# Optimization experiments

Measured on AMD Instinct MI355X. Metric: run time of the kernel, lower is better.

Reference implementation:

```python
import jax, jax.numpy as jnp
import numpy as np

B, L, D = 8, 1024, 512
H, Qd = 8, 64  # heads, per-head dim (q == v == 64)


def setup_inputs() -> dict:
    key = jax.random.key(0)
    ks = jax.random.split(key, 12)
    s = 0.02
    return {
        "x": jax.random.normal(ks[0], (B, L, D), dtype=jnp.float32),
        # Conv1d(D, D, kernel_size=1) == pointwise linear over channels
        "Wc": jax.random.normal(ks[1], (D, D), dtype=jnp.float32) * s,
        "bc": jax.random.normal(ks[2], (D,), dtype=jnp.float32) * s,
        "Wq": jax.random.normal(ks[3], (H * Qd, D), dtype=jnp.float32) * s,
        "bq": jax.random.normal(ks[4], (H * Qd,), dtype=jnp.float32) * s,
        "Wk": jax.random.normal(ks[5], (H * Qd, D), dtype=jnp.float32) * s,
        "bk": jax.random.normal(ks[6], (H * Qd,), dtype=jnp.float32) * s,
        "Wv": jax.random.normal(ks[7], (H * Qd, D), dtype=jnp.float32) * s,
        "bv": jax.random.normal(ks[8], (H * Qd,), dtype=jnp.float32) * s,
        "Wo": jax.random.normal(ks[9], (D, H * Qd), dtype=jnp.float32) * s,
        "bo": jax.random.normal(ks[10], (D,), dtype=jnp.float32) * s,
    }


def reference(x, Wc, bc, Wq, bq, Wk, bk, Wv, bv, Wo, bo):
    b, l, d = x.shape
    # kernel-size-1 Conv1d over channel dim == per-position linear
    x_r = jnp.einsum('bld,od->blo', x, Wc) + bc  # [B, L, D], Lr == L
    Q = (x @ Wq.T + bq).reshape(b, l, H, Qd).transpose(0, 2, 1, 3)    # bhld
    K = (x_r @ Wk.T + bk).reshape(b, l, H, Qd).transpose(0, 2, 1, 3)  # bhjd
    V = (x_r @ Wv.T + bv).reshape(b, l, H, Qd).transpose(0, 2, 1, 3)  # bhjd
    scores = jax.nn.softmax(
        jnp.einsum('bhld,bhjd->bhlj', Q, K) / np.sqrt(Qd).astype(np.float32),
        axis=-1)  # [B, H, L, L] — returned explicitly, must be materialized
    atten = jnp.einsum('bhlj,bhjd->bhld', scores, V)
    # NB: original flattens as (d, h), not the usual (h, d)
    merged = atten.transpose(0, 2, 3, 1).reshape(b, l, H * Qd)
    out = merged @ Wo.T + bo  # [B, L, D]
    return (out, scores)
```

## Files before the change

### kernel.cpp

```cpp
#include <hip/hip_runtime.h>
#include <stdint.h>

#define DEV __device__ __forceinline__

typedef __attribute__((ext_vector_type(8))) short short8;
typedef __attribute__((ext_vector_type(4))) float floatx4;

DEV ushort f2bf(float f) {
  union { float f; uint32_t u; } v; v.f = f;
  uint32_t u = v.u;
  return (ushort)((u + 0x7fffu + ((u >> 16) & 1u)) >> 16);
}

DEV float bf2f(ushort u) {
  union { uint32_t u; float f; } v; v.u = ((uint32_t)u) << 16;
  return v.f;
}

DEV floatx4 zero4() { floatx4 v; v[0] = 0.f; v[1] = 0.f; v[2] = 0.f; v[3] = 0.f; return v; }

__global__ __launch_bounds__(256) void cast_all(
    const float* __restrict__ x,
    const float* __restrict__ Wc, const float* __restrict__ Wq,
    const float* __restrict__ Wk, const float* __restrict__ Wv,
    const float* __restrict__ Wo,
    ushort* __restrict__ xb,
    ushort* __restrict__ Wcb, ushort* __restrict__ Wqb,
    ushort* __restrict__ Wkb, ushort* __restrict__ Wvb,
    ushort* __restrict__ Wob)
{
  const int y = blockIdx.y;
  const int i4 = blockIdx.x * 256 + threadIdx.x;
  if (y == 0) {
    if (i4 >= 1048576) return;
    float4 v = ((const float4*)x)[i4];
    ushort4 o;
    o.x = f2bf(v.x); o.y = f2bf(v.y); o.z = f2bf(v.z); o.w = f2bf(v.w);
    *(ushort4*)&xb[i4 * 4] = o;
  } else if (y <= 4) {
    if (i4 >= 65536) return;
    const float* s = (y == 1) ? Wc : (y == 2) ? Wq : (y == 3) ? Wk : Wv;
    ushort* d = (y == 1) ? Wcb : (y == 2) ? Wqb : (y == 3) ? Wkb : Wvb;
    float4 v = ((const float4*)s)[i4];
    ushort4 o;
    o.x = f2bf(v.x); o.y = f2bf(v.y); o.z = f2bf(v.z); o.w = f2bf(v.w);
    *(ushort4*)&d[i4 * 4] = o;
  } else {
    if (i4 >= 65536) return;
    int base = i4 * 4;
    #pragma unroll
    for (int k = 0; k < 4; k++) {
      int e = base + k;
      int o = e >> 9;
      int hd = e & 511;
      int h = hd >> 6, qd = hd & 63;
      Wob[e] = f2bf(Wo[o * 512 + qd * 8 + h]);
    }
  }
}

template <typename OutT>
__global__ __launch_bounds__(256) void gemm_bias(
    const ushort* __restrict__ A, int lda,
    const ushort* __restrict__ W,
    const float* __restrict__ bias0, const float* __restrict__ bias1,
    OutT* __restrict__ C, int ldc)
{
  __shared__ ushort As[64 * 40];
  __shared__ ushort Bs[64 * 40];

  const int t = threadIdx.x;
  const int lane = t & 63, w = t >> 6;
  const int ln = lane & 15, q = lane >> 4;
  const int row0 = blockIdx.y * 64, col0 = blockIdx.x * 64;
  const int wm = w >> 1, wn = w & 1;

  floatx4 acc[2][2];
  #pragma unroll
  for (int i = 0; i < 2; i++)
    #pragma unroll
    for (int j = 0; j < 2; j++) acc[i][j] = zero4();

  const int sr = t >> 2, ss = t & 3;
  for (int k0 = 0; k0 < 512; k0 += 32) {
    *(short8*)&As[sr * 40 + ss * 8] =
        *(const short8*)&A[(size_t)(row0 + sr) * lda + k0 + ss * 8];
    *(short8*)&Bs[sr * 40 + ss * 8] =
        *(const short8*)&W[(size_t)(col0 + sr) * 512 + k0 + ss * 8];
    __syncthreads();
    short8 af[2], bf[2];
    #pragma unroll
    for (int mi = 0; mi < 2; mi++)
      af[mi] = *(const short8*)&As[(wm * 32 + mi * 16 + ln) * 40 + q * 8];
    #pragma unroll
    for (int ni = 0; ni < 2; ni++)
      bf[ni] = *(const short8*)&Bs[(wn * 32 + ni * 16 + ln) * 40 + q * 8];
    #pragma unroll
    for (int mi = 0; mi < 2; mi++)
      #pragma unroll
      for (int ni = 0; ni < 2; ni++)
        acc[mi][ni] = __builtin_amdgcn_mfma_f32_16x16x32_bf16(
            af[mi], bf[ni], acc[mi][ni], 0, 0, 0);
    __syncthreads();
  }

  #pragma unroll
  for (int mi = 0; mi < 2; mi++)
    #pragma unroll
    for (int ni = 0; ni < 2; ni++) {
      int gcol = col0 + wn * 32 + ni * 16 + ln;
      float bv = (gcol < 512) ? bias0[gcol] : bias1[gcol - 512];
      #pragma unroll
      for (int r = 0; r < 4; r++) {
        int grow = row0 + wm * 32 + mi * 16 + q * 4 + r;
        float val = acc[mi][ni][r] + bv;
        if constexpr (sizeof(OutT) == 2) {
          C[(size_t)grow * ldc + gcol] = (OutT)f2bf(val);
        } else {
          C[(size_t)grow * ldc + gcol] = (OutT)val;
        }
      }
    }
}

__global__ __launch_bounds__(256) void vtrans(
    const ushort* __restrict__ KV, ushort* __restrict__ Vt)
{
  __shared__ ushort Ts[64 * 72];
  const int t = threadIdx.x;
  const int lt = blockIdx.x, pair = blockIdx.y;
  const int b = pair >> 3, h = pair & 7;
  #pragma unroll
  for (int i = 0; i < 2; i++) {
    int e = t + i * 256;
    int r = e >> 3, s = e & 7;
    *(short8*)&Ts[r * 72 + s * 8] =
        *(const short8*)&KV[((size_t)b * 1024 + lt * 64 + r) * 1024 + 512 + h * 64 + s * 8];
  }
  __syncthreads();
  #pragma unroll
  for (int i = 0; i < 2; i++) {
    int e = t + i * 256;
    int d = e >> 3, s = e & 7;
    short8 o;
    #pragma unroll
    for (int k = 0; k < 8; k++) o[k] = (short)Ts[(s * 8 + k) * 72 + d];
    *(short8*)&Vt[((size_t)pair * 64 + d) * 1024 + lt * 64 + s * 8] = o;
  }
}

__global__ __launch_bounds__(512) void attn(
    const ushort* __restrict__ XQ,
    const ushort* __restrict__ KV,
    const ushort* __restrict__ Vt,
    float* __restrict__ scores,
    ushort* __restrict__ Ab)
{
  __shared__ ushort Stage[128 * 72];
  __shared__ ushort Ps[32 * 136];
  __shared__ float sm[128];
  __shared__ float sl[128];

  const int t = threadIdx.x;
  const int lane = t & 63, w = t >> 6;
  const int ln = lane & 15, q = lane >> 4;
  const int wr = w >> 2, wc = w & 3;
  const int rt = blockIdx.x, pair = blockIdx.y;
  const int b = pair >> 3, h = pair & 7;
  const int l0 = rt * 32;
  const size_t bRow = (size_t)b * 1024;

  const ushort* qrow = &XQ[(bRow + l0 + wr * 16 + ln) * 1024 + 512 + h * 64];
  short8 a0 = *(const short8*)&qrow[q * 8];
  short8 a1 = *(const short8*)&qrow[32 + q * 8];

  floatx4 S[16];
  #pragma unroll
  for (int i = 0; i < 16; i++) S[i] = zero4();

  for (int ch = 0; ch < 8; ch++) {
    #pragma unroll
    for (int i = 0; i < 2; i++) {
      int e = t + i * 512;
      int r = e >> 3, s = e & 7;
      *(short8*)&Stage[r * 72 + s * 8] =
          *(const short8*)&KV[(bRow + ch * 128 + r) * 1024 + h * 64 + s * 8];
    }
    __syncthreads();
    #pragma unroll
    for (int sub = 0; sub < 2; sub++) {
      int jr = (wc + sub * 4) * 16;
      short8 b0 = *(const short8*)&Stage[(jr + ln) * 72 + q * 8];
      short8 b1 = *(const short8*)&Stage[(jr + ln) * 72 + 32 + q * 8];
      int ct = ch * 2 + sub;
      S[ct] = __builtin_amdgcn_mfma_f32_16x16x32_bf16(a0, b0, S[ct], 0, 0, 0);
      S[ct] = __builtin_amdgcn_mfma_f32_16x16x32_bf16(a1, b1, S[ct], 0, 0, 0);
    }
    __syncthreads();
  }

  float mr[4];
  #pragma unroll
  for (int r = 0; r < 4; r++) {
    float m = -3.4e38f;
    #pragma unroll
    for (int ct = 0; ct < 16; ct++) m = fmaxf(m, S[ct][r]);
    #pragma unroll
    for (int off = 1; off < 16; off <<= 1) m = fmaxf(m, __shfl_xor(m, off));
    mr[r] = m;
  }
  if (ln == 0) {
    #pragma unroll
    for (int r = 0; r < 4; r++) sm[wr * 64 + wc * 16 + q * 4 + r] = mr[r];
  }
  __syncthreads();
  float mfull[4], lsum[4];
  #pragma unroll
  for (int r = 0; r < 4; r++) {
    int base = wr * 64 + q * 4 + r;
    mfull[r] = fmaxf(fmaxf(sm[base], sm[base + 16]),
                     fmaxf(sm[base + 32], sm[base + 48]));
    lsum[r] = 0.0f;
  }
  #pragma unroll
  for (int ct = 0; ct < 16; ct++)
    #pragma unroll
    for (int r = 0; r < 4; r++) {
      float e = __expf((S[ct][r] - mfull[r]) * 0.125f);
      S[ct][r] = e;
      lsum[r] += e;
    }
  #pragma unroll
  for (int r = 0; r < 4; r++) {
    #pragma unroll
    for (int off = 1; off < 16; off <<= 1) lsum[r] += __shfl_xor(lsum[r], off);
  }
  if (ln == 0) {
    #pragma unroll
    for (int r = 0; r < 4; r++) sl[wr * 64 + wc * 16 + q * 4 + r] = lsum[r];
  }
  __syncthreads();
  float rl[4];
  #pragma unroll
  for (int r = 0; r < 4; r++) {
    int base = wr * 64 + q * 4 + r;
    rl[r] = 1.0f / (sl[base] + sl[base + 16] + sl[base + 32] + sl[base + 48]);
  }

  floatx4 O = zero4();
  const int srow = t >> 4;
  const int scb = (t & 15) * 8;
  for (int ch = 0; ch < 8; ch++) {
    #pragma unroll
    for (int i = 0; i < 2; i++) {
      int e = t + i * 512;
      int r = e >> 4, s = e & 15;
      *(short8*)&Stage[r * 136 + s * 8] =
          *(const short8*)&Vt[((size_t)pair * 64 + r) * 1024 + ch * 128 + s * 8];
    }
    #pragma unroll
    for (int sub = 0; sub < 2; sub++) {
      int ct = ch * 2 + sub;
      int c0 = (wc + sub * 4) * 16;
      #pragma unroll
      for (int r = 0; r < 4; r++)
        Ps[(wr * 16 + q * 4 + r) * 136 + c0 + ln] = f2bf(S[ct][r] * rl[r]);
    }
    __syncthreads();
    {
      short8 pv = *(const short8*)&Ps[srow * 136 + scb];
      size_t so = ((size_t)pair * 1024 + l0 + srow) * 1024 + ch * 128 + scb;
      float4 f0, f1;
      f0.x = bf2f((ushort)pv[0]); f0.y = bf2f((ushort)pv[1]);
      f0.z = bf2f((ushort)pv[2]); f0.w = bf2f((ushort)pv[3]);
      f1.x = bf2f((ushort)pv[4]); f1.y = bf2f((ushort)pv[5]);
      f1.z = bf2f((ushort)pv[6]); f1.w = bf2f((ushort)pv[7]);
      *(float4*)&scores[so] = f0;
      *(float4*)&scores[so + 4] = f1;
    }
    #pragma unroll
    for (int kc = 0; kc < 4; kc++) {
      short8 af = *(const short8*)&Ps[(wr * 16 + ln) * 136 + kc * 32 + q * 8];
      short8 bf = *(const short8*)&Stage[(wc * 16 + ln) * 136 + kc * 32 + q * 8];
      O = __builtin_amdgcn_mfma_f32_16x16x32_bf16(af, bf, O, 0, 0, 0);
    }
    __syncthreads();
  }

  #pragma unroll
  for (int r = 0; r < 4; r++) {
    Ab[(bRow + l0 + wr * 16 + q * 4 + r) * 512 + h * 64 + wc * 16 + ln] = f2bf(O[r]);
  }
}

extern "C" void kernel_launch(void* const* d_in, const int* in_sizes, int n_in,
                              void* d_out, int out_size, void* d_ws, size_t ws_size,
                              hipStream_t stream)
{
  const float* x  = (const float*)d_in[0];
  const float* Wc = (const float*)d_in[1];
  const float* bc = (const float*)d_in[2];
  const float* Wq = (const float*)d_in[3];
  const float* bq = (const float*)d_in[4];
  const float* Wk = (const float*)d_in[5];
  const float* bk = (const float*)d_in[6];
  const float* Wv = (const float*)d_in[7];
  const float* bv = (const float*)d_in[8];
  const float* Wo = (const float*)d_in[9];
  const float* bo = (const float*)d_in[10];

  float* out = (float*)d_out;
  float* scores = out + (size_t)8 * 1024 * 512;

  char* ws = (char*)d_ws;
  const size_t MB = (size_t)1 << 20;
  ushort* xb  = (ushort*)(ws + 0);
  ushort* Ab  = xb;
  ushort* XQ  = (ushort*)(ws + 8 * MB);
  ushort* KV  = (ushort*)(ws + 24 * MB);
  ushort* Vt  = (ushort*)(ws + 40 * MB);
  ushort* W1  = (ushort*)(ws + 48 * MB);
  ushort* W2  = (ushort*)(ws + 49 * MB);
  ushort* Wob = (ushort*)(ws + 50 * MB);

  cast_all<<<dim3(4096, 6), 256, 0, stream>>>(
      x, Wc, Wq, Wk, Wv, Wo,
      xb, W1, W1 + 262144, W2, W2 + 262144, Wob);

  gemm_bias<ushort><<<dim3(16, 128), 256, 0, stream>>>(
      xb, 512, W1, bc, bq, XQ, 1024);
  gemm_bias<ushort><<<dim3(16, 128), 256, 0, stream>>>(
      XQ, 1024, W2, bk, bv, KV, 1024);

  vtrans<<<dim3(16, 64), 256, 0, stream>>>(KV, Vt);

  attn<<<dim3(32, 64), 512, 0, stream>>>(XQ, KV, Vt, scores, Ab);

  gemm_bias<float><<<dim3(8, 128), 256, 0, stream>>>(
      Ab, 512, Wob, bo, bo, out, 512);
}
```

Before: 429.6 us.

## Retile GEMMs to 128x128 with swizzled LDS and restructure attention to direct-load K/V

The GEMM kernel moves to 128x128 tiles with a 64-wide K step and XOR-swizzled shared memory, giving more reuse per load and fewer bank conflicts. The attention kernel drops LDS staging for K and V and reads them straight from global memory into MFMA operands. It writes fp32 scores directly with nontemporal stores, before bf16 rounding, and keeps the full probability row block in a swizzled 64KB LDS buffer. Grid order is swapped so blocks sharing a head run together, and the cast kernel uses a flat grid with no idle blocks. The larger LDS footprint in attention lowers occupancy, and uncoalesced direct K/V loads may cost bandwidth.

```diff
diff --git a/kernel.cpp b/kernel.cpp
--- a/kernel.cpp
+++ b/kernel.cpp
@@ -10,11 +10,6 @@
   union { float f; uint32_t u; } v; v.f = f;
   uint32_t u = v.u;
   return (ushort)((u + 0x7fffu + ((u >> 16) & 1u)) >> 16);
-}
-
-DEV float bf2f(ushort u) {
-  union { uint32_t u; float f; } v; v.u = ((uint32_t)u) << 16;
-  return v.f;
 }
 
 DEV floatx4 zero4() { floatx4 v; v[0] = 0.f; v[1] = 0.f; v[2] = 0.f; v[3] = 0.f; return v; }
@@ -29,16 +24,20 @@
     ushort* __restrict__ Wkb, ushort* __restrict__ Wvb,
     ushort* __restrict__ Wob)
 {
-  const int y = blockIdx.y;
-  const int i4 = blockIdx.x * 256 + threadIdx.x;
+  const int bx = blockIdx.x;
+  int y, i4;
+  if (bx < 4096) { y = 0; i4 = bx * 256 + threadIdx.x; }
+  else {
+    int e = bx - 4096;
+    y = 1 + (e >> 8);
+    i4 = (e & 255) * 256 + threadIdx.x;
+  }
   if (y == 0) {
-    if (i4 >= 1048576) return;
     float4 v = ((const float4*)x)[i4];
     ushort4 o;
     o.x = f2bf(v.x); o.y = f2bf(v.y); o.z = f2bf(v.z); o.w = f2bf(v.w);
     *(ushort4*)&xb[i4 * 4] = o;
   } else if (y <= 4) {
-    if (i4 >= 65536) return;
     const float* s = (y == 1) ? Wc : (y == 2) ? Wq : (y == 3) ? Wk : Wv;
     ushort* d = (y == 1) ? Wcb : (y == 2) ? Wqb : (y == 3) ? Wkb : Wvb;
     float4 v = ((const float4*)s)[i4];
@@ -46,7 +45,6 @@
     o.x = f2bf(v.x); o.y = f2bf(v.y); o.z = f2bf(v.z); o.w = f2bf(v.w);
     *(ushort4*)&d[i4 * 4] = o;
   } else {
-    if (i4 >= 65536) return;
     int base = i4 * 4;
     #pragma unroll
     for (int k = 0; k < 4; k++) {
@@ -66,53 +64,67 @@
     const float* __restrict__ bias0, const float* __restrict__ bias1,
     OutT* __restrict__ C, int ldc)
 {
-  __shared__ ushort As[64 * 40];
-  __shared__ ushort Bs[64 * 40];
+  __shared__ __align__(16) ushort As[128 * 64];
+  __shared__ __align__(16) ushort Bs[128 * 64];
 
   const int t = threadIdx.x;
-  const int lane = t & 63, w = t >> 6;
+  const int lane = t & 63;
   const int ln = lane & 15, q = lane >> 4;
-  const int row0 = blockIdx.y * 64, col0 = blockIdx.x * 64;
+  const int w = t >> 6;
   const int wm = w >> 1, wn = w & 1;
-
-  floatx4 acc[2][2];
-  #pragma unroll
-  for (int i = 0; i < 2; i++)
-    #pragma unroll
-    for (int j = 0; j < 2; j++) acc[i][j] = zero4();
-
-  const int sr = t >> 2, ss = t & 3;
-  for (int k0 = 0; k0 < 512; k0 += 32) {
-    *(short8*)&As[sr * 40 + ss * 8] =
-        *(const short8*)&A[(size_t)(row0 + sr) * lda + k0 + ss * 8];
-    *(short8*)&Bs[sr * 40 + ss * 8] =
-        *(const short8*)&W[(size_t)(col0 + sr) * 512 + k0 + ss * 8];
+  const int row0 = blockIdx.x * 128, col0 = blockIdx.y * 128;
+
+  floatx4 acc[4][4];
+  #pragma unroll
+  for (int i = 0; i < 4; i++)
+    #pragma unroll
+    for (int j = 0; j < 4; j++) acc[i][j] = zero4();
+
+  const char* asb = (const char*)As;
+  const char* bsb = (const char*)Bs;
+
+  for (int k0 = 0; k0 < 512; k0 += 64) {
+    #pragma unroll
+    for (int i = 0; i < 4; i++) {
+      int L = i * 256 + t;
+      int r = L >> 3, s = L & 7;
+      int sg = s ^ (r & 7);
+      *(short8*)&As[L * 8] = *(const short8*)&A[(size_t)(row0 + r) * lda + k0 + sg * 8];
+      *(short8*)&Bs[L * 8] = *(const short8*)&W[(size_t)(col0 + r) * 512 + k0 + sg * 8];
+    }
     __syncthreads();
-    short8 af[2], bf[2];
-    #pragma unroll
-    for (int mi = 0; mi < 2; mi++)
-      af[mi] = *(const short8*)&As[(wm * 32 + mi * 16 + ln) * 40 + q * 8];
-    #pragma unroll
-    for (int ni = 0; ni < 2; ni++)
-      bf[ni] = *(const short8*)&Bs[(wn * 32 + ni * 16 + ln) * 40 + q * 8];
-    #pragma unroll
-    for (int mi = 0; mi < 2; mi++)
+    #pragma unroll
+    for (int kk = 0; kk < 2; kk++) {
+      short8 af[4], bf[4];
       #pragma unroll
-      for (int ni = 0; ni < 2; ni++)
-        acc[mi][ni] = __builtin_amdgcn_mfma_f32_16x16x32_bf16(
-            af[mi], bf[ni], acc[mi][ni], 0, 0, 0);
+      for (int mi = 0; mi < 4; mi++) {
+        int row = wm * 64 + mi * 16 + ln;
+        af[mi] = *(const short8*)(asb + ((row * 128 + kk * 64 + q * 16) ^ ((row & 7) << 4)));
+      }
+      #pragma unroll
+      for (int ni = 0; ni < 4; ni++) {
+        int row = wn * 64 + ni * 16 + ln;
+        bf[ni] = *(const short8*)(bsb + ((row * 128 + kk * 64 + q * 16) ^ ((row & 7) << 4)));
+      }
+      #pragma unroll
+      for (int mi = 0; mi < 4; mi++)
+        #pragma unroll
+        for (int ni = 0; ni < 4; ni++)
+          acc[mi][ni] = __builtin_amdgcn_mfma_f32_16x16x32_bf16(
+              af[mi], bf[ni], acc[mi][ni], 0, 0, 0);
+    }
     __syncthreads();
   }
 
   #pragma unroll
-  for (int mi = 0; mi < 2; mi++)
-    #pragma unroll
-    for (int ni = 0; ni < 2; ni++) {
-      int gcol = col0 + wn * 32 + ni * 16 + ln;
+  for (int mi = 0; mi < 4; mi++)
+    #pragma unroll
+    for (int ni = 0; ni < 4; ni++) {
+      int gcol = col0 + wn * 64 + ni * 16 + ln;
       float bv = (gcol < 512) ? bias0[gcol] : bias1[gcol - 512];
       #pragma unroll
       for (int r = 0; r < 4; r++) {
-        int grow = row0 + wm * 32 + mi * 16 + q * 4 + r;
+        int grow = row0 + wm * 64 + mi * 16 + q * 4 + r;
         float val = acc[mi][ni][r] + bv;
         if constexpr (sizeof(OutT) == 2) {
           C[(size_t)grow * ldc + gcol] = (OutT)f2bf(val);
@@ -126,7 +138,7 @@
 __global__ __launch_bounds__(256) void vtrans(
     const ushort* __restrict__ KV, ushort* __restrict__ Vt)
 {
-  __shared__ ushort Ts[64 * 72];
+  __shared__ __align__(16) ushort Ts[64 * 72];
   const int t = threadIdx.x;
   const int lt = blockIdx.x, pair = blockIdx.y;
   const int b = pair >> 3, h = pair & 7;
@@ -156,8 +168,7 @@
     float* __restrict__ scores,
     ushort* __restrict__ Ab)
 {
-  __shared__ ushort Stage[128 * 72];
-  __shared__ ushort Ps[32 * 136];
+  __shared__ __align__(16) ushort Ps[32 * 1024];
   __shared__ float sm[128];
   __shared__ float sl[128];
 
@@ -165,7 +176,7 @@
   const int lane = t & 63, w = t >> 6;
   const int ln = lane & 15, q = lane >> 4;
   const int wr = w >> 2, wc = w & 3;
-  const int rt = blockIdx.x, pair = blockIdx.y;
+  const int pair = blockIdx.x, rt = blockIdx.y;
   const int b = pair >> 3, h = pair & 7;
   const int l0 = rt * 32;
   const size_t bRow = (size_t)b * 1024;
@@ -178,25 +189,14 @@
   #pragma unroll
   for (int i = 0; i < 16; i++) S[i] = zero4();
 
-  for (int ch = 0; ch < 8; ch++) {
-    #pragma unroll
-    for (int i = 0; i < 2; i++) {
-      int e = t + i * 512;
-      int r = e >> 3, s = e & 7;
-      *(short8*)&Stage[r * 72 + s * 8] =
-          *(const short8*)&KV[(bRow + ch * 128 + r) * 1024 + h * 64 + s * 8];
-    }
-    __syncthreads();
-    #pragma unroll
-    for (int sub = 0; sub < 2; sub++) {
-      int jr = (wc + sub * 4) * 16;
-      short8 b0 = *(const short8*)&Stage[(jr + ln) * 72 + q * 8];
-      short8 b1 = *(const short8*)&Stage[(jr + ln) * 72 + 32 + q * 8];
-      int ct = ch * 2 + sub;
-      S[ct] = __builtin_amdgcn_mfma_f32_16x16x32_bf16(a0, b0, S[ct], 0, 0, 0);
-      S[ct] = __builtin_amdgcn_mfma_f32_16x16x32_bf16(a1, b1, S[ct], 0, 0, 0);
-    }
-    __syncthreads();
+  const ushort* krow = &KV[(bRow + wc * 16 + ln) * 1024 + h * 64];
+  #pragma unroll
+  for (int ct = 0; ct < 16; ct++) {
+    const ushort* kp = krow + (size_t)ct * 64 * 1024;
+    short8 b0 = *(const short8*)&kp[q * 8];
+    short8 b1 = *(const short8*)&kp[32 + q * 8];
+    S[ct] = __builtin_amdgcn_mfma_f32_16x16x32_bf16(a0, b0, S[ct], 0, 0, 0);
+    S[ct] = __builtin_amdgcn_mfma_f32_16x16x32_bf16(a1, b1, S[ct], 0, 0, 0);
   }
 
   float mr[4];
@@ -247,49 +247,41 @@
     rl[r] = 1.0f / (sl[base] + sl[base + 16] + sl[base + 32] + sl[base + 48]);
   }
 
-  floatx4 O = zero4();
-  const int srow = t >> 4;
-  const int scb = (t & 15) * 8;
-  for (int ch = 0; ch < 8; ch++) {
-    #pragma unroll
-    for (int i = 0; i < 2; i++) {
-      int e = t + i * 512;
-      int r = e >> 4, s = e & 15;
-      *(short8*)&Stage[r * 136 + s * 8] =
-          *(const short8*)&Vt[((size_t)pair * 64 + r) * 1024 + ch * 128 + s * 8];
-    }
-    #pragma unroll
-    for (int sub = 0; sub < 2; sub++) {
-      int ct = ch * 2 + sub;
-      int c0 = (wc + sub * 4) * 16;
-      #pragma unroll
-      for (int r = 0; r < 4; r++)
-        Ps[(wr * 16 + q * 4 + r) * 136 + c0 + ln] = f2bf(S[ct][r] * rl[r]);
-    }
-    __syncthreads();
-    {
-      short8 pv = *(const short8*)&Ps[srow * 136 + scb];
-      size_t so = ((size_t)pair * 1024 + l0 + srow) * 1024 + ch * 128 + scb;
-      float4 f0, f1;
-      f0.x = bf2f((ushort)pv[0]); f0.y = bf2f((ushort)pv[1]);
-      f0.z = bf2f((ushort)pv[2]); f0.w = bf2f((ushort)pv[3]);
-      f1.x = bf2f((ushort)pv[4]); f1.y = bf2f((ushort)pv[5]);
-      f1.z = bf2f((ushort)pv[6]); f1.w = bf2f((ushort)pv[7]);
-      *(float4*)&scores[so] = f0;
-      *(float4*)&scores[so + 4] = f1;
-    }
-    #pragma unroll
-    for (int kc = 0; kc < 4; kc++) {
-      short8 af = *(const short8*)&Ps[(wr * 16 + ln) * 136 + kc * 32 + q * 8];
-      short8 bf = *(const short8*)&Stage[(wc * 16 + ln) * 136 + kc * 32 + q * 8];
-      O = __builtin_amdgcn_mfma_f32_16x16x32_bf16(af, bf, O, 0, 0, 0);
-    }
-    __syncthreads();
-  }
-
-  #pragma unroll
-  for (int r = 0; r < 4; r++) {
-    Ab[(bRow + l0 + wr * 16 + q * 4 + r) * 512 + h * 64 + wc * 16 + ln] = f2bf(O[r]);
+  char* psb = (char*)Ps;
+  #pragma unroll
+  for (int ct = 0; ct < 16; ct++) {
+    int col = ct * 64 + wc * 16 + ln;
+    #pragma unroll
+    for (int r = 0; r < 4; r++) {
+      int row = wr * 16 + q * 4 + r;
+      float p = S[ct][r] * rl[r];
+      __builtin_nontemporal_store(
+          p, &scores[((size_t)pair * 1024 + l0 + row) * 1024 + col]);
+      *(ushort*)(psb + (((row * 1024 + col) * 2) ^ ((row & 7) << 4))) = f2bf(p);
+    }
+  }
+  __syncthreads();
+
+  floatx4 O0 = zero4(), O1 = zero4();
+  const int arow = wr * 16 + ln;
+  const int aswz = (arow & 7) << 4;
+  const char* pa = psb + arow * 2048;
+  const ushort* vrow = &Vt[((size_t)pair * 64 + wc * 16 + ln) * 1024];
+  #pragma unroll
+  for (int kc2 = 0; kc2 < 16; kc2++) {
+    int k0 = kc2 * 2;
+    short8 af0 = *(const short8*)(pa + ((k0 * 64 + q * 16) ^ aswz));
+    short8 bv0 = *(const short8*)&vrow[k0 * 32 + q * 8];
+    O0 = __builtin_amdgcn_mfma_f32_16x16x32_bf16(af0, bv0, O0, 0, 0, 0);
+    short8 af1 = *(const short8*)(pa + (((k0 + 1) * 64 + q * 16) ^ aswz));
+    short8 bv1 = *(const short8*)&vrow[(k0 + 1) * 32 + q * 8];
+    O1 = __builtin_amdgcn_mfma_f32_16x16x32_bf16(af1, bv1, O1, 0, 0, 0);
+  }
+
+  #pragma unroll
+  for (int r = 0; r < 4; r++) {
+    float o = O0[r] + O1[r];
+    Ab[(bRow + l0 + wr * 16 + q * 4 + r) * 512 + h * 64 + wc * 16 + ln] = f2bf(o);
   }
 }
 
@@ -323,19 +315,19 @@
   ushort* W2  = (ushort*)(ws + 49 * MB);
   ushort* Wob = (ushort*)(ws + 50 * MB);
 
-  cast_all<<<dim3(4096, 6), 256, 0, stream>>>(
+  cast_all<<<dim3(4096 + 5 * 256), 256, 0, stream>>>(
       x, Wc, Wq, Wk, Wv, Wo,
       xb, W1, W1 + 262144, W2, W2 + 262144, Wob);
 
-  gemm_bias<ushort><<<dim3(16, 128), 256, 0, stream>>>(
+  gemm_bias<ushort><<<dim3(64, 8), 256, 0, stream>>>(
       xb, 512, W1, bc, bq, XQ, 1024);
-  gemm_bias<ushort><<<dim3(16, 128), 256, 0, stream>>>(
+  gemm_bias<ushort><<<dim3(64, 8), 256, 0, stream>>>(
       XQ, 1024, W2, bk, bv, KV, 1024);
 
   vtrans<<<dim3(16, 64), 256, 0, stream>>>(KV, Vt);
 
-  attn<<<dim3(32, 64), 512, 0, stream>>>(XQ, KV, Vt, scores, Ab);
-
-  gemm_bias<float><<<dim3(8, 128), 256, 0, stream>>>(
+  attn<<<dim3(64, 32), 512, 0, stream>>>(XQ, KV, Vt, scores, Ab);
+
+  gemm_bias<float><<<dim3(64, 4), 256, 0, stream>>>(
       Ab, 512, Wob, bo, bo, out, 512);
 }
```

Result: slower. 459.8 us (+7.0%).
